# Performance work log

Measured on AMD Instinct MI355X. Metric: run time of the kernel, lower is better.

The kernel has to match this reference:

```python
import jax, jax.numpy as jnp
import numpy as np

DIM = 1024
NUM_EXPERTS = 8
TOP_K = 2


def setup_inputs() -> dict:
    key = jax.random.key(0)
    ks = jax.random.split(key, 7)
    s_in = 1.0 / np.sqrt(DIM)
    s_hid = 1.0 / np.sqrt(4 * DIM)
    x = jax.random.normal(ks[0], (2, 2048, DIM), dtype=jnp.float32)
    gate_w = jax.random.normal(ks[1], (DIM, NUM_EXPERTS), dtype=jnp.float32) * s_in
    gate_b = jax.random.normal(ks[2], (NUM_EXPERTS,), dtype=jnp.float32) * 0.01
    w1 = jax.random.normal(ks[3], (NUM_EXPERTS, DIM, 4 * DIM), dtype=jnp.float32) * s_in
    b1 = jax.random.normal(ks[4], (NUM_EXPERTS, 4 * DIM), dtype=jnp.float32) * 0.01
    w2 = jax.random.normal(ks[5], (NUM_EXPERTS, 4 * DIM, DIM), dtype=jnp.float32) * s_hid
    b2 = jax.random.normal(ks[6], (NUM_EXPERTS, DIM), dtype=jnp.float32) * 0.01
    return {"x": x, "gate_w": gate_w, "gate_b": gate_b, "w1": w1, "b1": b1, "w2": w2, "b2": b2}


def reference(x, gate_w, gate_b, w1, b1, w2, b2):
    # Faithful to the torch module in EVAL mode (no routing noise).
    # Quirks reproduced: (1) gather of expert inputs degenerates to flat_x
    # (all top_k copies identical); (2) softmax-normalized gates are dead code
    # (never applied); (3) the per-expert masked assignment overwrites all
    # TOP_K. Net: out = TOP_K * FFN_{max(topk_idx)}(x).
    B, N, C = x.shape
    flat_x = x.reshape(-1, C)                      # [T, C]
    logits = flat_x @ gate_w + gate_b              # [T, E]
    _, topk_idx = jax.lax.top_k(logits, TOP_K)     # [T, k]
    e_star = jnp.max(topk_idx, axis=-1)            # [T] last-overwriting expert
    out = jnp.zeros_like(flat_x)
    for i in range(NUM_EXPERTS):                   # fixed small expert loop
        h = jax.nn.gelu(flat_x @ w1[i] + b1[i], approximate=False)  # exact GELU (torch default)
        y = h @ w2[i] + b2[i]                      # [T, C]
        out = jnp.where((e_star == i)[:, None], y, out)
    return (TOP_K * out).reshape(B, N, C)
```

## Files before the change

kernel.cpp:

```cpp
#include <hip/hip_runtime.h>
#include <hip/hip_bf16.h>
#include <hip/hip_fp16.h>

#define T_TOKENS 4096
#define DIMC 1024
#define HID 4096
#define NE 8

typedef _Float16 f16;
typedef _Float16 f16x8 __attribute__((ext_vector_type(8)));
typedef _Float16 f16x4 __attribute__((ext_vector_type(4)));
typedef float f32x4 __attribute__((ext_vector_type(4)));

__device__ __forceinline__ void gload_lds16(const f16* g, f16* l) {
    __builtin_amdgcn_global_load_lds(
        (const __attribute__((address_space(1))) void*)g,
        (__attribute__((address_space(3))) void*)l, 16, 0, 0);
}

__global__ __launch_bounds__(256) void gating_kernel(
    const float* __restrict__ x, const float* __restrict__ gw,
    const float* __restrict__ gb, int* __restrict__ counts,
    int* __restrict__ list)
{
    const int wave = threadIdx.x >> 6;
    const int lane = threadIdx.x & 63;
    const int t = blockIdx.x * 4 + wave;

    const float* xr = x + (size_t)t * DIMC;
    float acc[NE];
#pragma unroll
    for (int e = 0; e < NE; ++e) acc[e] = 0.f;

    for (int i = 0; i < DIMC / 64; ++i) {
        const int k = i * 64 + lane;
        const float xv = xr[k];
        const float* g = gw + (size_t)k * NE;
#pragma unroll
        for (int e = 0; e < NE; ++e) acc[e] = fmaf(xv, g[e], acc[e]);
    }
#pragma unroll
    for (int off = 32; off >= 1; off >>= 1) {
#pragma unroll
        for (int e = 0; e < NE; ++e) acc[e] += __shfl_xor(acc[e], off, 64);
    }
    if (lane == 0) {
        float lg[NE];
#pragma unroll
        for (int e = 0; e < NE; ++e) lg[e] = acc[e] + gb[e];
        int i1 = 0; float v1 = lg[0];
#pragma unroll
        for (int e = 1; e < NE; ++e) { if (lg[e] > v1) { v1 = lg[e]; i1 = e; } }
        int i2 = -1; float v2 = -3.4e38f;
#pragma unroll
        for (int e = 0; e < NE; ++e) {
            if (e == i1) continue;
            if (lg[e] > v2) { v2 = lg[e]; i2 = e; }
        }
        const int es = (i1 > i2) ? i1 : i2;
        const int pos = atomicAdd(&counts[es], 1);
        list[es * T_TOKENS + pos] = t;
    }
}

__global__ __launch_bounds__(256) void xconvert(const float* __restrict__ x,
                                                f16* __restrict__ xh)
{
    const size_t i = ((size_t)blockIdx.x * 256 + threadIdx.x) * 8;
    const float4 a = *(const float4*)(x + i);
    const float4 b = *(const float4*)(x + i + 4);
    f16x8 v;
    v[0] = (f16)a.x; v[1] = (f16)a.y; v[2] = (f16)a.z; v[3] = (f16)a.w;
    v[4] = (f16)b.x; v[5] = (f16)b.y; v[6] = (f16)b.z; v[7] = (f16)b.w;
    *(f16x8*)(xh + i) = v;
}

__global__ __launch_bounds__(256) void wconvert(const float* __restrict__ W,
                                                f16* __restrict__ Wt,
                                                int K, int N)
{
    __shared__ f16 Lt[64 * 72];
    const int n0 = blockIdx.x * 64;
    const int k0 = blockIdx.y * 64;
    const float* Ws = W + (size_t)blockIdx.z * K * N;
    const int t = threadIdx.x;

    const int no = (t & 15) * 4;
    const int kr = t >> 4;
#pragma unroll
    for (int p = 0; p < 4; ++p) {
        const int k = kr + p * 16;
        const float4 v = *(const float4*)(Ws + (size_t)(k0 + k) * N + n0 + no);
        Lt[(no + 0) * 72 + k] = (f16)v.x;
        Lt[(no + 1) * 72 + k] = (f16)v.y;
        Lt[(no + 2) * 72 + k] = (f16)v.z;
        Lt[(no + 3) * 72 + k] = (f16)v.w;
    }
    __syncthreads();
    const int n = t >> 2;
    const int ko = (t & 3) * 16;
    const f16x8 a = *(const f16x8*)&Lt[n * 72 + ko];
    const f16x8 b = *(const f16x8*)&Lt[n * 72 + ko + 8];
    f16* dst = Wt + ((size_t)blockIdx.z * N + n0 + n) * K + k0 + ko;
    *(f16x8*)(dst) = a;
    *(f16x8*)(dst + 8) = b;
}

template <bool FIRST>
__global__ __launch_bounds__(256) void ffn_gemm3(
    const f16* __restrict__ A, const f16* __restrict__ Bt,
    const float* __restrict__ bias, const int* __restrict__ counts,
    const int* __restrict__ list, f16* __restrict__ Hout,
    float* __restrict__ out)
{
    constexpr int KB   = FIRST ? DIMC : HID;
    constexpr int NTOT = FIRST ? HID : DIMC;
    constexpr int NKT  = 16;

    const int e   = FIRST ? (int)blockIdx.z : (int)(blockIdx.z >> 2);
    const int ks  = FIRST ? 0 : (int)(blockIdx.z & 3);
    const int kk0 = ks * 1024;
    const int m0  = blockIdx.y * 128;
    const int n0  = blockIdx.x * 128;
    const int cnt = counts[e];
    if (m0 >= cnt) return;

    __shared__ __align__(16) f16 As[128 * 64];
    __shared__ __align__(16) f16 Bs[128 * 64];
    __shared__ int rows[128];

    const int tid = threadIdx.x;
    if (tid < 128) rows[tid] = (m0 + tid < cnt) ? list[e * T_TOKENS + m0 + tid] : -1;
    __syncthreads();

    const int lane = tid & 63;
    const int wv   = tid >> 6;
    const int wr   = wv >> 1, wc = wv & 1;

    const f16* asrc[4];
    const f16* bsrc[4];
    f16* adst[4];
    f16* bdst[4];
#pragma unroll
    for (int j = 0; j < 4; ++j) {
        const int row   = wv * 32 + j * 8 + (lane >> 3);
        const int chunk = (lane & 7) ^ (row & 7);
        int tok = rows[row]; if (tok < 0) tok = 0;
        asrc[j] = A + (size_t)tok * KB + kk0 + chunk * 8;
        bsrc[j] = Bt + ((size_t)e * NTOT + n0 + row) * KB + kk0 + chunk * 8;
        adst[j] = As + (wv * 32 + j * 8) * 64;
        bdst[j] = Bs + (wv * 32 + j * 8) * 64;
    }

    f32x4 acc[4][4];
#pragma unroll
    for (int mi = 0; mi < 4; ++mi)
#pragma unroll
        for (int ni = 0; ni < 4; ++ni) acc[mi][ni] = f32x4{0.f, 0.f, 0.f, 0.f};

    for (int kt = 0; kt < NKT; ++kt) {
        const int ko = kt * 64;
        __syncthreads();
#pragma unroll
        for (int j = 0; j < 4; ++j) {
            gload_lds16(asrc[j] + ko, adst[j]);
            gload_lds16(bsrc[j] + ko, bdst[j]);
        }
        __syncthreads();
#pragma unroll
        for (int kh = 0; kh < 2; ++kh) {
            f16x8 af[4], bf[4];
#pragma unroll
            for (int mi = 0; mi < 4; ++mi) {
                const int row = wr * 64 + mi * 16 + (lane & 15);
                const int kb  = (((lane >> 4) * 16) + kh * 64) ^ ((row & 7) << 4);
                af[mi] = *(const f16x8*)((const char*)As + row * 128 + kb);
            }
#pragma unroll
            for (int ni = 0; ni < 4; ++ni) {
                const int n  = wc * 64 + ni * 16 + (lane & 15);
                const int kb = (((lane >> 4) * 16) + kh * 64) ^ ((n & 7) << 4);
                bf[ni] = *(const f16x8*)((const char*)Bs + n * 128 + kb);
            }
#pragma unroll
            for (int mi = 0; mi < 4; ++mi)
#pragma unroll
                for (int ni = 0; ni < 4; ++ni)
                    acc[mi][ni] = __builtin_amdgcn_mfma_f32_16x16x32_f16(
                        af[mi], bf[ni], acc[mi][ni], 0, 0, 0);
        }
    }

#pragma unroll
    for (int ni = 0; ni < 4; ++ni) {
        const int gc = n0 + wc * 64 + ni * 16 + (lane & 15);
        const float bv = FIRST ? bias[(size_t)e * HID + gc]
                               : ((ks == 0) ? 2.f * bias[(size_t)e * DIMC + gc] : 0.f);
#pragma unroll
        for (int mi = 0; mi < 4; ++mi) {
#pragma unroll
            for (int r = 0; r < 4; ++r) {
                const int lrow = wr * 64 + mi * 16 + (lane >> 4) * 4 + r;
                const int tok = rows[lrow];
                if (tok < 0) continue;
                if (FIRST) {
                    const float v = acc[mi][ni][r] + bv;
                    const float g = 0.5f * v * (1.f + erff(v * 0.70710678118f));
                    Hout[(size_t)tok * HID + gc] = (f16)g;
                } else {
                    atomicAdd(out + (size_t)tok * DIMC + gc,
                              2.f * acc[mi][ni][r] + bv);
                }
            }
        }
    }
}

template <bool FIRST>
__global__ __launch_bounds__(256) void ffn_gemm_fb(
    const float* __restrict__ x, const f16* __restrict__ Hin,
    const float* __restrict__ w1, const float* __restrict__ b1,
    const float* __restrict__ w2, const float* __restrict__ b2,
    const int* __restrict__ counts, const int* __restrict__ list,
    f16* __restrict__ Hout, float* __restrict__ out)
{
    constexpr int K = FIRST ? DIMC : HID;
    constexpr int N = FIRST ? HID : DIMC;
    constexpr int LDT = 40;

    const int e  = blockIdx.z;
    const int m0 = blockIdx.y * 128;
    const int n0 = blockIdx.x * 128;
    const int cnt = counts[e];
    if (m0 >= cnt) return;

    __shared__ f16 Ab[128 * LDT];
    __shared__ f16 Bb[128 * LDT];
    __shared__ int rows[128];

    const int tid = threadIdx.x;
    if (tid < 128) {
        const int p = m0 + tid;
        rows[tid] = (p < cnt) ? list[e * T_TOKENS + p] : -1;
    }
    __syncthreads();

    const int lane = tid & 63;
    const int wv = tid >> 6;
    const int wr = wv >> 1, wc = wv & 1;

    f32x4 acc[4][4];
#pragma unroll
    for (int mi = 0; mi < 4; ++mi)
#pragma unroll
        for (int ni = 0; ni < 4; ++ni) acc[mi][ni] = f32x4{0.f, 0.f, 0.f, 0.f};

    const float* Bsrc = (FIRST ? w1 : w2) + (size_t)e * K * N;

    for (int kk = 0; kk < K; kk += 32) {
        __syncthreads();
        {
            const int r  = tid >> 3;
            const int ko = (tid & 7) * 4;
#pragma unroll
            for (int p = 0; p < 4; ++p) {
                const int row = p * 32 + r;
                const int tok = rows[row];
                f16x4 hv;
                if (FIRST) {
                    float4 v;
                    if (tok >= 0) v = *(const float4*)(x + (size_t)tok * K + kk + ko);
                    else          v = make_float4(0.f, 0.f, 0.f, 0.f);
                    hv[0] = (f16)v.x; hv[1] = (f16)v.y; hv[2] = (f16)v.z; hv[3] = (f16)v.w;
                } else {
                    if (tok >= 0) hv = *(const f16x4*)(Hin + (size_t)tok * K + kk + ko);
                    else { hv[0] = (f16)0.f; hv[1] = (f16)0.f; hv[2] = (f16)0.f; hv[3] = (f16)0.f; }
                }
                *(f16x4*)&Ab[row * LDT + ko] = hv;
            }
        }
        {
            const int kb = tid >> 5;
            const int no = (tid & 31) * 4;
#pragma unroll
            for (int p = 0; p < 4; ++p) {
                const int k = p * 8 + kb;
                const float4 v = *(const float4*)(Bsrc + (size_t)(kk + k) * N + n0 + no);
                f16 h[4];
                h[0] = (f16)v.x; h[1] = (f16)v.y; h[2] = (f16)v.z; h[3] = (f16)v.w;
#pragma unroll
                for (int i = 0; i < 4; ++i) {
                    const int n = no + i;
                    const int chunk = (k >> 3) ^ ((n >> 2) & 3);
                    Bb[n * LDT + chunk * 8 + (k & 7)] = h[i];
                }
            }
        }
        __syncthreads();
        f16x8 af[4], bf[4];
#pragma unroll
        for (int mi = 0; mi < 4; ++mi) {
            const int row = wr * 64 + mi * 16 + (lane & 15);
            af[mi] = *(const f16x8*)&Ab[row * LDT + (lane >> 4) * 8];
        }
#pragma unroll
        for (int ni = 0; ni < 4; ++ni) {
            const int n = wc * 64 + ni * 16 + (lane & 15);
            const int chunk = (lane >> 4) ^ ((n >> 2) & 3);
            bf[ni] = *(const f16x8*)&Bb[n * LDT + chunk * 8];
        }
#pragma unroll
        for (int mi = 0; mi < 4; ++mi)
#pragma unroll
            for (int ni = 0; ni < 4; ++ni)
                acc[mi][ni] = __builtin_amdgcn_mfma_f32_16x16x32_f16(
                    af[mi], bf[ni], acc[mi][ni], 0, 0, 0);
    }

#pragma unroll
    for (int ni = 0; ni < 4; ++ni) {
        const int gc = n0 + wc * 64 + ni * 16 + (lane & 15);
        const float bias = FIRST ? b1[(size_t)e * HID + gc]
                                 : b2[(size_t)e * DIMC + gc];
#pragma unroll
        for (int mi = 0; mi < 4; ++mi) {
#pragma unroll
            for (int r = 0; r < 4; ++r) {
                const int lrow = wr * 64 + mi * 16 + (lane >> 4) * 4 + r;
                const int tok = rows[lrow];
                if (tok < 0) continue;
                const float v = acc[mi][ni][r] + bias;
                if (FIRST) {
                    const float g = 0.5f * v * (1.f + erff(v * 0.70710678118f));
                    Hout[(size_t)tok * HID + gc] = (f16)g;
                } else {
                    out[(size_t)tok * DIMC + gc] = 2.f * v;
                }
            }
        }
    }
}

extern "C" void kernel_launch(void* const* d_in, const int* in_sizes, int n_in,
                              void* d_out, int out_size, void* d_ws, size_t ws_size,
                              hipStream_t stream)
{
    const float* x   = (const float*)d_in[0];
    const float* gw  = (const float*)d_in[1];
    const float* gb  = (const float*)d_in[2];
    const float* w1  = (const float*)d_in[3];
    const float* b1  = (const float*)d_in[4];
    const float* w2  = (const float*)d_in[5];
    const float* b2  = (const float*)d_in[6];
    float* out = (float*)d_out;

    const size_t MB = 1 << 20;
    const size_t need_big = 169 * MB;

    if (ws_size >= need_big) {
        int* counts = (int*)d_ws;
        int* list   = (int*)((char*)d_ws + 1024);
        f16* xh     = (f16*)((char*)d_ws + 1 * MB);
        f16* H      = (f16*)((char*)d_ws + 9 * MB);
        f16* w1t    = (f16*)((char*)d_ws + 41 * MB);
        f16* w2t    = (f16*)((char*)d_ws + 105 * MB);

        hipMemsetAsync(counts, 0, 1024, stream);
        hipMemsetAsync(out, 0, (size_t)T_TOKENS * DIMC * sizeof(float), stream);

        gating_kernel<<<T_TOKENS / 4, 256, 0, stream>>>(x, gw, gb, counts, list);
        xconvert<<<(T_TOKENS * DIMC) / (256 * 8), 256, 0, stream>>>(x, xh);
        wconvert<<<dim3(HID / 64, DIMC / 64, NE), 256, 0, stream>>>(w1, w1t, DIMC, HID);
        wconvert<<<dim3(DIMC / 64, HID / 64, NE), 256, 0, stream>>>(w2, w2t, HID, DIMC);

        ffn_gemm3<true><<<dim3(HID / 128, T_TOKENS / 128, NE), 256, 0, stream>>>(
            xh, w1t, b1, counts, list, H, nullptr);
        ffn_gemm3<false><<<dim3(DIMC / 128, T_TOKENS / 128, NE * 4), 256, 0, stream>>>(
            H, w2t, b2, counts, list, nullptr, out);
        return;
    }

    const size_t need_fb = (size_t)(1 << 18) + (size_t)T_TOKENS * HID * sizeof(f16);
    if (ws_size < need_fb) return;

    int* counts = (int*)d_ws;
    int* list   = (int*)((char*)d_ws + 1024);
    f16* H      = (f16*)((char*)d_ws + (1 << 18));

    hipMemsetAsync(d_ws, 0, 1024, stream);
    gating_kernel<<<T_TOKENS / 4, 256, 0, stream>>>(x, gw, gb, counts, list);
    ffn_gemm_fb<true><<<dim3(HID / 128, T_TOKENS / 128, NE), 256, 0, stream>>>(
        x, (const f16*)nullptr, w1, b1, w2, b2, counts, list, H, out);
    ffn_gemm_fb<false><<<dim3(DIMC / 128, T_TOKENS / 128, NE), 256, 0, stream>>>(
        x, (const f16*)H, w1, b1, w2, b2, counts, list, H, out);
}
```

Before: 370.5 us.

## Split first GEMM over K and replace output atomics with partial-sum reduction

The first expert GEMM is split into two K-halves to double grid parallelism. It writes fp16 partial sums that a new gelu_combine kernel adds, biases and passes through exact GELU. The second GEMM stores its four K-split partials to a workspace buffer instead of doing atomicAdd into the output, and a reduce4 kernel sums them, which also removes the output memset. This trades atomics and low occupancy for extra memory traffic, two extra launches and a larger workspace requirement. Storing the first-layer partials in fp16 before the bias and GELU adds a small precision loss.

```diff
diff --git a/kernel.cpp b/kernel.cpp
--- a/kernel.cpp
+++ b/kernel.cpp
@@ -21,7 +21,7 @@
 __global__ __launch_bounds__(256) void gating_kernel(
     const float* __restrict__ x, const float* __restrict__ gw,
     const float* __restrict__ gb, int* __restrict__ counts,
-    int* __restrict__ list)
+    int* __restrict__ list, int* __restrict__ eidx)
 {
     const int wave = threadIdx.x >> 6;
     const int lane = threadIdx.x & 63;
@@ -60,6 +60,7 @@
         const int es = (i1 > i2) ? i1 : i2;
         const int pos = atomicAdd(&counts[es], 1);
         list[es * T_TOKENS + pos] = t;
+        eidx[t] = es;
     }
 }
 
@@ -107,19 +108,21 @@
 }
 
 template <bool FIRST>
-__global__ __launch_bounds__(256) void ffn_gemm3(
+__global__ __launch_bounds__(256) void ffn_gemm7(
     const f16* __restrict__ A, const f16* __restrict__ Bt,
     const float* __restrict__ bias, const int* __restrict__ counts,
-    const int* __restrict__ list, f16* __restrict__ Hout,
-    float* __restrict__ out)
+    const int* __restrict__ list, f16* __restrict__ Hp,
+    float* __restrict__ pout)
 {
     constexpr int KB   = FIRST ? DIMC : HID;
     constexpr int NTOT = FIRST ? HID : DIMC;
-    constexpr int NKT  = 16;
-
-    const int e   = FIRST ? (int)blockIdx.z : (int)(blockIdx.z >> 2);
-    const int ks  = FIRST ? 0 : (int)(blockIdx.z & 3);
-    const int kk0 = ks * 1024;
+    constexpr int NKT  = FIRST ? 8 : 16;
+    constexpr int KCH  = FIRST ? 512 : 1024;
+
+    const int zz  = blockIdx.z;
+    const int e   = FIRST ? (zz >> 1) : (zz >> 2);
+    const int ks  = FIRST ? (zz & 1) : (zz & 3);
+    const int kk0 = ks * KCH;
     const int m0  = blockIdx.y * 128;
     const int n0  = blockIdx.x * 128;
     const int cnt = counts[e];
@@ -194,7 +197,7 @@
 #pragma unroll
     for (int ni = 0; ni < 4; ++ni) {
         const int gc = n0 + wc * 64 + ni * 16 + (lane & 15);
-        const float bv = FIRST ? bias[(size_t)e * HID + gc]
+        const float bv = FIRST ? 0.f
                                : ((ks == 0) ? 2.f * bias[(size_t)e * DIMC + gc] : 0.f);
 #pragma unroll
         for (int mi = 0; mi < 4; ++mi) {
@@ -204,16 +207,54 @@
                 const int tok = rows[lrow];
                 if (tok < 0) continue;
                 if (FIRST) {
-                    const float v = acc[mi][ni][r] + bv;
-                    const float g = 0.5f * v * (1.f + erff(v * 0.70710678118f));
-                    Hout[(size_t)tok * HID + gc] = (f16)g;
+                    Hp[((size_t)ks * T_TOKENS + tok) * HID + gc] =
+                        (f16)acc[mi][ni][r];
                 } else {
-                    atomicAdd(out + (size_t)tok * DIMC + gc,
-                              2.f * acc[mi][ni][r] + bv);
+                    pout[((size_t)ks * T_TOKENS + tok) * DIMC + gc] =
+                        2.f * acc[mi][ni][r] + bv;
                 }
             }
         }
     }
+}
+
+__global__ __launch_bounds__(256) void gelu_combine(
+    const f16* __restrict__ Hp, const float* __restrict__ b1,
+    const int* __restrict__ eidx, f16* __restrict__ H)
+{
+    const size_t i = ((size_t)blockIdx.x * 256 + threadIdx.x) * 8;
+    const int t = (int)(i >> 12);
+    const int c = (int)(i & (HID - 1));
+    const int e = eidx[t];
+    const f16x8 a = *(const f16x8*)(Hp + i);
+    const f16x8 b = *(const f16x8*)(Hp + (size_t)T_TOKENS * HID + i);
+    const float4 ba = *(const float4*)(b1 + (size_t)e * HID + c);
+    const float4 bb = *(const float4*)(b1 + (size_t)e * HID + c + 4);
+    const float bj[8] = {ba.x, ba.y, ba.z, ba.w, bb.x, bb.y, bb.z, bb.w};
+    f16x8 o;
+#pragma unroll
+    for (int j = 0; j < 8; ++j) {
+        const float v = (float)a[j] + (float)b[j] + bj[j];
+        o[j] = (f16)(0.5f * v * (1.f + erff(v * 0.70710678118f)));
+    }
+    *(f16x8*)(H + i) = o;
+}
+
+__global__ __launch_bounds__(256) void reduce4(const float* __restrict__ p,
+                                               float* __restrict__ out)
+{
+    constexpr size_t SL = (size_t)T_TOKENS * DIMC;
+    const size_t i = ((size_t)blockIdx.x * 256 + threadIdx.x) * 4;
+    const float4 a = *(const float4*)(p + i);
+    const float4 b = *(const float4*)(p + SL + i);
+    const float4 c = *(const float4*)(p + 2 * SL + i);
+    const float4 d = *(const float4*)(p + 3 * SL + i);
+    float4 s;
+    s.x = a.x + b.x + c.x + d.x;
+    s.y = a.y + b.y + c.y + d.y;
+    s.z = a.z + b.z + c.z + d.z;
+    s.w = a.w + b.w + c.w + d.w;
+    *(float4*)(out + i) = s;
 }
 
 template <bool FIRST>
@@ -355,28 +396,32 @@
     float* out = (float*)d_out;
 
     const size_t MB = 1 << 20;
-    const size_t need_big = 169 * MB;
-
-    if (ws_size >= need_big) {
+    const size_t need_p = 233 * MB;
+
+    if (ws_size >= need_p) {
         int* counts = (int*)d_ws;
         int* list   = (int*)((char*)d_ws + 1024);
+        int* eidx   = (int*)((char*)d_ws + 512 * 1024);
         f16* xh     = (f16*)((char*)d_ws + 1 * MB);
         f16* H      = (f16*)((char*)d_ws + 9 * MB);
         f16* w1t    = (f16*)((char*)d_ws + 41 * MB);
         f16* w2t    = (f16*)((char*)d_ws + 105 * MB);
+        f16* Hp     = (f16*)((char*)d_ws + 169 * MB);
+        float* p    = (float*)((char*)d_ws + 169 * MB);
 
         hipMemsetAsync(counts, 0, 1024, stream);
-        hipMemsetAsync(out, 0, (size_t)T_TOKENS * DIMC * sizeof(float), stream);
-
-        gating_kernel<<<T_TOKENS / 4, 256, 0, stream>>>(x, gw, gb, counts, list);
+
+        gating_kernel<<<T_TOKENS / 4, 256, 0, stream>>>(x, gw, gb, counts, list, eidx);
         xconvert<<<(T_TOKENS * DIMC) / (256 * 8), 256, 0, stream>>>(x, xh);
         wconvert<<<dim3(HID / 64, DIMC / 64, NE), 256, 0, stream>>>(w1, w1t, DIMC, HID);
         wconvert<<<dim3(DIMC / 64, HID / 64, NE), 256, 0, stream>>>(w2, w2t, HID, DIMC);
 
-        ffn_gemm3<true><<<dim3(HID / 128, T_TOKENS / 128, NE), 256, 0, stream>>>(
-            xh, w1t, b1, counts, list, H, nullptr);
-        ffn_gemm3<false><<<dim3(DIMC / 128, T_TOKENS / 128, NE * 4), 256, 0, stream>>>(
-            H, w2t, b2, counts, list, nullptr, out);
+        ffn_gemm7<true><<<dim3(HID / 128, T_TOKENS / 128, NE * 2), 256, 0, stream>>>(
+            xh, w1t, nullptr, counts, list, Hp, nullptr);
+        gelu_combine<<<(T_TOKENS * HID) / (256 * 8), 256, 0, stream>>>(Hp, b1, eidx, H);
+        ffn_gemm7<false><<<dim3(DIMC / 128, T_TOKENS / 128, NE * 4), 256, 0, stream>>>(
+            H, w2t, b2, counts, list, nullptr, p);
+        reduce4<<<(T_TOKENS * DIMC) / (256 * 4), 256, 0, stream>>>(p, out);
         return;
     }
 
@@ -385,10 +430,11 @@
 
     int* counts = (int*)d_ws;
     int* list   = (int*)((char*)d_ws + 1024);
+    int* eidx   = (int*)((char*)d_ws + 160 * 1024);
     f16* H      = (f16*)((char*)d_ws + (1 << 18));
 
     hipMemsetAsync(d_ws, 0, 1024, stream);
-    gating_kernel<<<T_TOKENS / 4, 256, 0, stream>>>(x, gw, gb, counts, list);
+    gating_kernel<<<T_TOKENS / 4, 256, 0, stream>>>(x, gw, gb, counts, list, eidx);
     ffn_gemm_fb<true><<<dim3(HID / 128, T_TOKENS / 128, NE), 256, 0, stream>>>(
         x, (const f16*)nullptr, w1, b1, w2, b2, counts, list, H, out);
     ffn_gemm_fb<false><<<dim3(DIMC / 128, T_TOKENS / 128, NE), 256, 0, stream>>>(
```

Result: faster. 341.6 us (-7.8%).
